# Optimization experiments

Measured on AMD Instinct MI355X. Metric: run time of the kernel, lower is better.

## Reference

```python
import jax, jax.numpy as jnp
import numpy as np

B, S, H = 2, 2048, 2048
NH, NKV, D = 16, 4, 128
E, K, F = 16, 2, 768
EPS = 1e-6
THETA = 1e6


def setup_inputs() -> dict:
    key = jax.random.key(0)
    ks = jax.random.split(key, 10)
    sd = 0.02
    rn = lambda k, shp: jax.random.normal(k, shp, jnp.float32) * sd
    return {
        "positions": jnp.arange(S, dtype=jnp.int32),
        "hidden_states": jax.random.normal(ks[0], (B, S, H), jnp.float32),
        "residual": jax.random.normal(ks[1], (B, S, H), jnp.float32),
        "w_in_ln": jnp.ones((H,), jnp.float32),
        "wq": rn(ks[2], (H, NH * D)),
        "wk": rn(ks[3], (H, NKV * D)),
        "wv": rn(ks[4], (H, NKV * D)),
        "wo": rn(ks[5], (NH * D, H)),
        "q_norm_w": jnp.ones((D,), jnp.float32),
        "k_norm_w": jnp.ones((D,), jnp.float32),
        "w_post_ln": jnp.ones((H,), jnp.float32),
        "gate_w": rn(ks[6], (H, E)),
        "w_gate_up": rn(ks[7], (E, H, 2 * F)),
        "w_down": rn(ks[8], (E, F, H)),
    }


def _rmsnorm(x, w):
    return x * jax.lax.rsqrt(jnp.mean(x * x, axis=-1, keepdims=True) + EPS) * w


def _rope(x, positions):
    # x: [B, S, h, D], neox-style rotate-half RoPE
    half = D // 2
    inv_freq = 1.0 / (THETA ** (jnp.arange(half, dtype=jnp.float32) / half))
    ang = positions.astype(jnp.float32)[:, None] * inv_freq  # [S, half]
    cos = jnp.cos(ang)[None, :, None, :]
    sin = jnp.sin(ang)[None, :, None, :]
    x1, x2 = x[..., :half], x[..., half:]
    return jnp.concatenate([x1 * cos - x2 * sin, x2 * cos + x1 * sin], axis=-1)


def reference(positions, hidden_states, residual, w_in_ln, wq, wk, wv, wo,
              q_norm_w, k_norm_w, w_post_ln, gate_w, w_gate_up, w_down):
    # fused RMSNorm + residual (residual is not None branch)
    residual = hidden_states + residual
    h = _rmsnorm(residual, w_in_ln)

    # --- Qwen3 attention: qk-norm + RoPE + causal GQA ---
    q = _rmsnorm((h @ wq).reshape(B, S, NH, D), q_norm_w)
    k = _rmsnorm((h @ wk).reshape(B, S, NKV, D), k_norm_w)
    v = (h @ wv).reshape(B, S, NKV, D)
    q = _rope(q, positions)
    k = _rope(k, positions)
    rep = NH // NKV
    k = jnp.repeat(k, rep, axis=2)
    v = jnp.repeat(v, rep, axis=2)
    scores = jnp.einsum('bqhd,bkhd->bhqk', q, k) / np.sqrt(D).astype(np.float32)
    causal = jnp.tril(jnp.ones((S, S), bool))
    scores = jnp.where(causal, scores, -jnp.inf)
    attn = jax.nn.softmax(scores, axis=-1)
    o = jnp.einsum('bhqk,bkhd->bqhd', attn, v).reshape(B, S, NH * D) @ wo

    # fused RMSNorm + residual
    residual = o + residual
    h = _rmsnorm(residual, w_post_ln)

    # --- MoE: top-k router (renormalized) + capacity-based grouped GEMM dispatch ---
    x = h.reshape(-1, H)                      # [T, H]
    T = B * S
    probs = jax.nn.softmax((x @ gate_w).astype(jnp.float32), axis=-1)
    tw, tids = jax.lax.top_k(probs, K)        # [T, K]
    tw = (tw / tw.sum(axis=-1, keepdims=True)).astype(x.dtype)

    P = T * K
    C = (2 * P) // E
    eids = tids.reshape(-1)                   # [P]
    oneh = jax.nn.one_hot(eids, E, dtype=jnp.int32)
    pos_in_e = (jnp.cumsum(oneh, axis=0) * oneh).sum(-1) - 1   # slot within expert
    valid = pos_in_e < C
    pos_c = jnp.minimum(pos_in_e, C - 1)
    e_safe = jnp.where(valid, eids, E)        # overflow -> dump row E

    xr = jnp.repeat(x, K, axis=0)             # [P, H]
    buf = jnp.zeros((E + 1, C, H), x.dtype).at[e_safe, pos_c].set(xr)[:E]
    gu = jnp.einsum('ech,ehf->ecf', buf, w_gate_up)            # [E, C, 2F]
    g, u = jnp.split(gu, 2, axis=-1)
    dn = jnp.einsum('ecf,efh->ech', jax.nn.silu(g) * u, w_down)
    dn = jnp.concatenate([dn, jnp.zeros((1, C, H), dn.dtype)], axis=0)
    yp = dn[e_safe, pos_c] * tw.reshape(-1)[:, None]           # [P, H]
    y = yp.reshape(T, K, H).sum(axis=1)
    return y.reshape(B, S, H), residual
```

## Files before the change

### kernel.cpp

```cpp
#include <hip/hip_runtime.h>
#include <stdint.h>

#define T_TOK 4096
#define HDIM  2048
#define SEQ   2048
#define NHQ   16
#define NKVH  4
#define DH    128
#define NE    16
#define CCAP  1024
#define FF    768
#define EPSF  1e-6f

typedef __attribute__((ext_vector_type(4))) float          f32x4;
typedef __attribute__((ext_vector_type(8))) _Float16       f16x8;
typedef __attribute__((ext_vector_type(4))) unsigned short u16x4;
typedef __attribute__((ext_vector_type(8))) unsigned short u16x8;

__device__ __forceinline__ unsigned short f2h(float f){ return __builtin_bit_cast(unsigned short, (_Float16)f); }
__device__ __forceinline__ float h2f(unsigned short u){ return (float)__builtin_bit_cast(_Float16, u); }
__device__ __forceinline__ void split2(float x, unsigned short& hi, unsigned short& lo){
  unsigned short h = f2h(x);
  hi = h; lo = f2h((x - h2f(h)) * 4096.f);
}
__device__ __forceinline__ void gl_lds16(const void* g, void* l){
  __builtin_amdgcn_global_load_lds((const __attribute__((address_space(1))) unsigned int*)g,
                                   (__attribute__((address_space(3))) unsigned int*)l, 16, 0, 0);
}
__device__ __forceinline__ int bswz(int row){ return ((row & 7) ^ ((row >> 3) & 7)) << 3; }

__global__ __launch_bounds__(256) void k_addnorm(
    const float* __restrict__ hs, const float* __restrict__ rs, const float* __restrict__ w,
    float* __restrict__ resid, unsigned short* __restrict__ hhi, unsigned short* __restrict__ hlo)
{
  int t = blockIdx.x, tid = threadIdx.x;
  size_t off = (size_t)t * HDIM;
  float4 a0 = ((const float4*)(hs+off))[tid];
  float4 b0 = ((const float4*)(rs+off))[tid];
  float4 a1 = ((const float4*)(hs+off))[tid+256];
  float4 b1 = ((const float4*)(rs+off))[tid+256];
  float4 s0 = make_float4(a0.x+b0.x, a0.y+b0.y, a0.z+b0.z, a0.w+b0.w);
  float4 s1 = make_float4(a1.x+b1.x, a1.y+b1.y, a1.z+b1.z, a1.w+b1.w);
  float ssq = s0.x*s0.x+s0.y*s0.y+s0.z*s0.z+s0.w*s0.w
            + s1.x*s1.x+s1.y*s1.y+s1.z*s1.z+s1.w*s1.w;
  #pragma unroll
  for (int sh=1; sh<64; sh<<=1) ssq += __shfl_xor(ssq, sh);
  __shared__ float red[4];
  if ((tid & 63) == 0) red[tid>>6] = ssq;
  __syncthreads();
  float tot = red[0]+red[1]+red[2]+red[3];
  float r = 1.f / sqrtf(tot * (1.f/HDIM) + EPSF);
  ((float4*)(resid+off))[tid]     = s0;
  ((float4*)(resid+off))[tid+256] = s1;
  float4 w0 = ((const float4*)w)[tid];
  float4 w1 = ((const float4*)w)[tid+256];
  u16x4 hv, lv; unsigned short ta, tb;
  split2(s0.x*r*w0.x, ta, tb); hv.x=ta; lv.x=tb;
  split2(s0.y*r*w0.y, ta, tb); hv.y=ta; lv.y=tb;
  split2(s0.z*r*w0.z, ta, tb); hv.z=ta; lv.z=tb;
  split2(s0.w*r*w0.w, ta, tb); hv.w=ta; lv.w=tb;
  ((u16x4*)(hhi+off))[tid] = hv; ((u16x4*)(hlo+off))[tid] = lv;
  split2(s1.x*r*w1.x, ta, tb); hv.x=ta; lv.x=tb;
  split2(s1.y*r*w1.y, ta, tb); hv.y=ta; lv.y=tb;
  split2(s1.z*r*w1.z, ta, tb); hv.z=ta; lv.z=tb;
  split2(s1.w*r*w1.w, ta, tb); hv.w=ta; lv.w=tb;
  ((u16x4*)(hhi+off))[tid+256] = hv; ((u16x4*)(hlo+off))[tid+256] = lv;
}

__global__ void k_cstab(const int* __restrict__ pos, float* __restrict__ cs)
{
  int i = blockIdx.x*256 + threadIdx.x;
  if (i >= SEQ*64) return;
  int s = i >> 6, f = i & 63;
  float pw  = (float)exp((double)f * 13.815510557964274 / 64.0);
  float inv = 1.0f / pw;
  float ang = (float)pos[s] * inv;
  float sv, cv;
  sincosf(ang, &sv, &cv);
  ((float2*)cs)[i] = make_float2(cv, sv);
}

__global__ __launch_bounds__(256) void k_normrope(
    unsigned short* __restrict__ qh, unsigned short* __restrict__ ql,
    unsigned short* __restrict__ kh, unsigned short* __restrict__ kl,
    const float* __restrict__ qnw, const float* __restrict__ knw,
    const float* __restrict__ cs)
{
  int t = blockIdx.x, head = blockIdx.y*4 + (threadIdx.x>>6), lane = threadIdx.x & 63;
  int s = t & (SEQ-1);
  unsigned short *dh, *dl; const float* wn; float scale; size_t off;
  if (head < NHQ){ off = ((size_t)t*NHQ + head)*DH; dh = qh+off; dl = ql+off; wn = qnw; scale = 0.08838834764831845f; }
  else           { off = ((size_t)t*NKVH + (head-NHQ))*DH; dh = kh+off; dl = kl+off; wn = knw; scale = 1.f; }
  float x1 = h2f(dh[lane])    + h2f(dl[lane])   *(1.f/4096.f);
  float x2 = h2f(dh[lane+64]) + h2f(dl[lane+64])*(1.f/4096.f);
  float ssq = x1*x1 + x2*x2;
  #pragma unroll
  for (int sh=1; sh<64; sh<<=1) ssq += __shfl_xor(ssq, sh);
  float r = 1.f / sqrtf(ssq * (1.f/DH) + EPSF);
  float y1 = x1*r*wn[lane], y2 = x2*r*wn[lane+64];
  float2 csp = ((const float2*)cs)[s*64 + lane];
  float o1 = (y1*csp.x - y2*csp.y) * scale;
  float o2 = (y2*csp.x + y1*csp.y) * scale;
  unsigned short a, b;
  split2(o1, a, b); dh[lane]    = a; dl[lane]    = b;
  split2(o2, a, b); dh[lane+64] = a; dl[lane+64] = b;
}

__global__ __launch_bounds__(256) void k_wsplit(
    const float* __restrict__ W, int Kd, int Ncols,
    unsigned short* __restrict__ Whi, unsigned short* __restrict__ Wlo)
{
  int k0 = blockIdx.x*64, n0 = blockIdx.y*64;
  __shared__ float T[64][65];
  int tid = threadIdx.x;
  int tr = tid >> 4;
  int tc = (tid & 15) * 4;
  #pragma unroll
  for (int i=0;i<4;i++){
    int k = tr + i*16;
    float4 v = *(const float4*)(W + (size_t)(k0 + k)*Ncols + n0 + tc);
    T[k][tc+0]=v.x; T[k][tc+1]=v.y; T[k][tc+2]=v.z; T[k][tc+3]=v.w;
  }
  __syncthreads();
  int n  = tid >> 2;
  int kc = (tid & 3) * 16;
  u16x8 hv0, lv0, hv1, lv1;
  #pragma unroll
  for (int j=0;j<8;j++){
    unsigned short hi, lo; split2(T[kc+j][n], hi, lo);
    hv0[j]=hi; lv0[j]=lo;
  }
  #pragma unroll
  for (int j=0;j<8;j++){
    unsigned short hi, lo; split2(T[kc+8+j][n], hi, lo);
    hv1[j]=hi; lv1[j]=lo;
  }
  size_t ob = (size_t)(n0 + n)*Kd + k0 + kc;
  *(u16x8*)(Whi + ob)     = hv0;
  *(u16x8*)(Whi + ob + 8) = hv1;
  *(u16x8*)(Wlo + ob)     = lv0;
  *(u16x8*)(Wlo + ob + 8) = lv1;
}

__global__ __launch_bounds__(256,2) void k_gemm_qkv(
    const unsigned short* __restrict__ Ahi, const unsigned short* __restrict__ Alo,
    const unsigned short* __restrict__ Whi, const unsigned short* __restrict__ Wlo,
    unsigned short* __restrict__ qh, unsigned short* __restrict__ ql,
    unsigned short* __restrict__ kh, unsigned short* __restrict__ kl,
    unsigned short* __restrict__ vh, unsigned short* __restrict__ vl)
{
  const int Kd = HDIM;
  int bm = blockIdx.x, bn2 = blockIdx.y;
  int bn, N, noff; unsigned short *Ch, *Cl;
  if (bn2 < 16){ bn = bn2;      N = 2048; noff = 0;    Ch = qh; Cl = ql; }
  else if (bn2 < 20){ bn = bn2-16; N = 512; noff = 2048; Ch = kh; Cl = kl; }
  else { bn = bn2-20; N = 512; noff = 2560; Ch = vh; Cl = vl; }

  __shared__ unsigned short As[2][8192];
  __shared__ unsigned short Bs[2][8192];

  int tid = threadIdx.x, lane = tid & 63, w = tid >> 6;
  int wr = w >> 1, wc = w & 1;

  size_t arow_g[4], brow_g[4];
  int lb_[4];
  #pragma unroll
  for (int i=0;i<4;i++){
    int ob = w*4096 + i*1024 + lane*16;
    int row = ob >> 7;
    int colB = ob & 127;
    int scolB = colB ^ ((row & 7) << 4);
    arow_g[i] = (size_t)(bm*128 + row) * Kd + (scolB >> 1);
    brow_g[i] = (size_t)(noff + bn*128 + row) * Kd + (scolB >> 1);
    lb_[i] = (w*4096 + i*1024) >> 1;
  }

  f32x4 accA[4][4] = {};
  f32x4 accB[4][4] = {};

  for (int kt = 0; kt < Kd/64; kt++){
    #pragma unroll
    for (int i=0;i<4;i++){
      gl_lds16(Ahi + arow_g[i] + kt*64, (void*)&As[0][lb_[i]]);
      gl_lds16(Alo + arow_g[i] + kt*64, (void*)&As[1][lb_[i]]);
      gl_lds16(Whi + brow_g[i] + kt*64, (void*)&Bs[0][lb_[i]]);
      gl_lds16(Wlo + brow_g[i] + kt*64, (void*)&Bs[1][lb_[i]]);
    }
    __syncthreads();
    #pragma unroll
    for (int kk=0; kk<2; kk++){
      f16x8 ah[4], al[4], bh[4], bl[4];
      #pragma unroll
      for (int m=0;m<4;m++){
        int row = wr*64 + m*16 + (lane & 15);
        int ci = (kk*32 + ((lane>>4)<<3)) ^ ((row & 7) << 3);
        ah[m] = *(const f16x8*)&As[0][row*64 + ci];
        al[m] = *(const f16x8*)&As[1][row*64 + ci];
      }
      #pragma unroll
      for (int n=0;n<4;n++){
        int row = wc*64 + n*16 + (lane & 15);
        int ci = (kk*32 + ((lane>>4)<<3)) ^ ((row & 7) << 3);
        bh[n] = *(const f16x8*)&Bs[0][row*64 + ci];
        bl[n] = *(const f16x8*)&Bs[1][row*64 + ci];
      }
      #pragma unroll
      for (int m=0;m<4;m++)
        #pragma unroll
        for (int n=0;n<4;n++){
          accA[m][n] = __builtin_amdgcn_mfma_f32_16x16x32_f16(ah[m], bh[n], accA[m][n], 0,0,0);
          accB[m][n] = __builtin_amdgcn_mfma_f32_16x16x32_f16(ah[m], bl[n], accB[m][n], 0,0,0);
          accB[m][n] = __builtin_amdgcn_mfma_f32_16x16x32_f16(al[m], bh[n], accB[m][n], 0,0,0);
        }
    }
    __syncthreads();
  }
  int r0 = (lane >> 4) << 2, c0 = lane & 15;
  #pragma unroll
  for (int m=0;m<4;m++){
    int grow0 = bm*128 + wr*64 + m*16 + r0;
    #pragma unroll
    for (int n=0;n<4;n++){
      int gcol = bn*128 + wc*64 + n*16 + c0;
      #pragma unroll
      for (int j=0;j<4;j++){
        float v = accA[m][n][j] + accB[m][n][j] * (1.f/4096.f);
        int grow = grow0 + j;
        unsigned short hi, lo; split2(v, hi, lo);
        Ch[(size_t)grow*N + gcol] = hi;
        Cl[(size_t)grow*N + gcol] = lo;
      }
    }
  }
}

template<int MODE>
__global__ __launch_bounds__(256,2) void k_gemm(
    const unsigned short* __restrict__ Ahi, const unsigned short* __restrict__ Alo,
    const float* __restrict__ Bsrc,
    const unsigned short* __restrict__ Bhi, const unsigned short* __restrict__ Blo,
    void* __restrict__ C1,
    int N, int Kd,
    const int* __restrict__ erow, const int* __restrict__ counts,
    const float* __restrict__ topw)
{
  constexpr int SPLIT = (MODE <= 2) ? 1 : 0;
  int bm = blockIdx.x, bn = blockIdx.y, e = blockIdx.z;
  int cnt = 0;
  const unsigned short* Abase = Ahi;
  const float* Bp = Bsrc;
  if constexpr (MODE == 3){ cnt = counts[e]; if (bm*128 >= cnt) return; Bp = Bsrc + (size_t)e*Kd*N; }
  if constexpr (MODE == 4){ cnt = counts[e]; if (bm*128 >= cnt) return; Bp = Bsrc + (size_t)e*Kd*N; Abase = Ahi + (size_t)e*CCAP*Kd; }

  __shared__ unsigned short As[SPLIT?2:1][8192];
  __shared__ unsigned short Bs[SPLIT?2:1][8192];

  int tid = threadIdx.x, lane = tid & 63, w = tid >> 6;
  int wr = w >> 1, wc = w & 1;

  size_t arow_g[4], brow_g[4];
  int lb_[4];
  #pragma unroll
  for (int i=0;i<4;i++){
    int ob = w*4096 + i*1024 + lane*16;
    int row = ob >> 7;
    int colB = ob & 127;
    int scolB = colB ^ ((row & 7) << 4);
    int grow;
    if constexpr (MODE == 3){
      grow = erow[e*CCAP + bm*128 + row] >> 1;
    } else {
      grow = bm*128 + row;
    }
    arow_g[i] = (size_t)grow * Kd + (scolB >> 1);
    brow_g[i] = (size_t)(bn*128 + row) * Kd + (scolB >> 1);
    lb_[i] = (w*4096 + i*1024) >> 1;
  }

  f32x4 accA[4][4] = {};
  f32x4 accB[4][4] = {};

  int nK = Kd >> 6;
  for (int kt = 0; kt < nK; kt++){
    #pragma unroll
    for (int i=0;i<4;i++){
      gl_lds16(Abase + arow_g[i] + kt*64, (void*)&As[0][lb_[i]]);
      if constexpr (SPLIT) gl_lds16(Alo + arow_g[i] + kt*64, (void*)&As[1][lb_[i]]);
    }
    if constexpr (SPLIT){
      #pragma unroll
      for (int i=0;i<4;i++){
        gl_lds16(Bhi + brow_g[i] + kt*64, (void*)&Bs[0][lb_[i]]);
        gl_lds16(Blo + brow_g[i] + kt*64, (void*)&Bs[1][lb_[i]]);
      }
    } else {
      #pragma unroll
      for (int it=0; it<2; it++){
        int b2 = tid + it*256;
        int k0 = (b2 >> 5) << 2;
        int n0 = (b2 & 31) << 2;
        const float* bp = Bp + (size_t)(kt*64 + k0)*N + bn*128 + n0;
        float4 f0 = *(const float4*)bp;
        float4 f1 = *(const float4*)(bp + (size_t)N);
        float4 f2 = *(const float4*)(bp + 2*(size_t)N);
        float4 f3 = *(const float4*)(bp + 3*(size_t)N);
        #define DO_COL(J, CX) { \
          int rown = n0 + J; \
          int idx = rown*64 + (k0 ^ bswz(rown)); \
          u16x4 ph; ph.x=f2h(f0.CX); ph.y=f2h(f1.CX); ph.z=f2h(f2.CX); ph.w=f2h(f3.CX); \
          *(u16x4*)&Bs[0][idx] = ph; }
        DO_COL(0, x) DO_COL(1, y) DO_COL(2, z) DO_COL(3, w)
        #undef DO_COL
      }
    }
    __syncthreads();
    #pragma unroll
    for (int kk=0; kk<2; kk++){
      f16x8 ah[4], al[4], bh[4], bl[4];
      #pragma unroll
      for (int m=0;m<4;m++){
        int row = wr*64 + m*16 + (lane & 15);
        int ci = (kk*32 + ((lane>>4)<<3)) ^ ((row & 7) << 3);
        ah[m] = *(const f16x8*)&As[0][row*64 + ci];
        if constexpr (SPLIT) al[m] = *(const f16x8*)&As[1][row*64 + ci];
      }
      #pragma unroll
      for (int n=0;n<4;n++){
        int row = wc*64 + n*16 + (lane & 15);
        int sw = SPLIT ? ((row & 7) << 3) : bswz(row);
        int ci = (kk*32 + ((lane>>4)<<3)) ^ sw;
        bh[n] = *(const f16x8*)&Bs[0][row*64 + ci];
        if constexpr (SPLIT) bl[n] = *(const f16x8*)&Bs[1][row*64 + ci];
      }
      #pragma unroll
      for (int m=0;m<4;m++)
        #pragma unroll
        for (int n=0;n<4;n++){
          accA[m][n] = __builtin_amdgcn_mfma_f32_16x16x32_f16(ah[m], bh[n], accA[m][n], 0,0,0);
          if constexpr (SPLIT){
            accB[m][n] = __builtin_amdgcn_mfma_f32_16x16x32_f16(ah[m], bl[n], accB[m][n], 0,0,0);
            accB[m][n] = __builtin_amdgcn_mfma_f32_16x16x32_f16(al[m], bh[n], accB[m][n], 0,0,0);
          }
        }
    }
    __syncthreads();
  }
  int r0 = (lane >> 4) << 2, c0 = lane & 15;
  #pragma unroll
  for (int m=0;m<4;m++){
    int grow0 = bm*128 + wr*64 + m*16 + r0;
    #pragma unroll
    for (int n=0;n<4;n++){
      int gcol = bn*128 + wc*64 + n*16 + c0;
      #pragma unroll
      for (int j=0;j<4;j++){
        float v = accA[m][n][j];
        if constexpr (SPLIT) v += accB[m][n][j] * (1.f/4096.f);
        int grow = grow0 + j;
        if constexpr (MODE == 2){
          size_t idx = (size_t)grow*N + gcol;
          ((float*)C1)[idx] += v;
        } else if constexpr (MODE == 3){
          ((unsigned short*)C1)[((size_t)e*CCAP + grow)*N + gcol] = f2h(v);
        } else if constexpr (MODE == 4){
          if (grow < cnt){
            int p = erow[e*CCAP + grow];
            ((float*)C1)[(size_t)p*N + gcol] = v;
          }
        }
      }
    }
  }
}

__global__ __launch_bounds__(512,2) void k_attn(
    const unsigned short* __restrict__ qh, const unsigned short* __restrict__ ql,
    const unsigned short* __restrict__ kh, const unsigned short* __restrict__ kl,
    const unsigned short* __restrict__ vh, const unsigned short* __restrict__ vl,
    unsigned short* __restrict__ oh, unsigned short* __restrict__ ol)
{
  int h = blockIdx.y, b = blockIdx.z;
  int qt = b ? (15 - blockIdx.x) : blockIdx.x;
  int hkv = h >> 2;
  int tid = threadIdx.x, lane = tid & 63, w = tid >> 6;

  __shared__ unsigned short Ks[2][2][8192];
  __shared__ unsigned short Vs[2][2][8192];
  __shared__ unsigned short Ps[8][2][1024];

  int qrow = qt*128 + w*16 + (lane & 15);
  size_t qoff = ((size_t)(b*SEQ + qrow)*NHQ + h)*DH + ((lane>>4)<<3);
  f16x8 qfh[4], qfl[4];
  #pragma unroll
  for (int kk=0; kk<4; kk++){
    qfh[kk] = *(const f16x8*)(qh + qoff + kk*32);
    qfl[kk] = *(const f16x8*)(ql + qoff + kk*32);
  }

  const size_t SROW = (size_t)NKVH*DH;
  size_t kvbase = (size_t)b*SEQ*SROW + (size_t)hkv*DH;
  int kob[2]; size_t koff[2];
  #pragma unroll
  for (int i=0;i<2;i++){
    int ob = i*8192 + tid*16;
    int row = ob >> 8;
    int scol = (ob & 255) ^ ((row & 7) << 4);
    kob[i] = ob;
    koff[i] = (size_t)row*SROW + (scol >> 1);
  }
  int vkvp = (tid & 31) * 2;
  int vd0  = ((tid >> 5) & 15) * 8;
  size_t voff0 = (size_t)vkvp*SROW + vd0;
  size_t voff1 = voff0 + SROW;

  u16x8 pkh[2], pkl[2];
  u16x8 pvh[2], pvl[2];

  #define STAGE_LOAD(KVT) { \
    size_t tb = kvbase + (size_t)(KVT)*64*SROW; \
    _Pragma("unroll") \
    for (int i=0;i<2;i++){ pkh[i] = *(const u16x8*)(kh + tb + koff[i]); \
                           pkl[i] = *(const u16x8*)(kl + tb + koff[i]); } \
    pvh[0] = *(const u16x8*)(vh + tb + voff0); \
    pvh[1] = *(const u16x8*)(vh + tb + voff1); \
    pvl[0] = *(const u16x8*)(vl + tb + voff0); \
    pvl[1] = *(const u16x8*)(vl + tb + voff1); }

  #define STAGE_WRITE(BUF) { \
    _Pragma("unroll") \
    for (int i=0;i<2;i++){ \
      *(u16x8*)((char*)&Ks[BUF][0][0] + kob[i]) = pkh[i]; \
      *(u16x8*)((char*)&Ks[BUF][1][0] + kob[i]) = pkl[i]; } \
    _Pragma("unroll") \
    for (int jj=0;jj<8;jj++){ \
      int row = vd0 + jj; \
      int idx = row*64 + (vkvp ^ ((jj & 7) << 3)); \
      *(unsigned int*)&Vs[BUF][0][idx] = (unsigned int)pvh[0][jj] | ((unsigned int)pvh[1][jj] << 16); \
      *(unsigned int*)&Vs[BUF][1][idx] = (unsigned int)pvl[0][jj] | ((unsigned int)pvl[1][jj] << 16); } }

  #define QKT(KVT, BUF) { \
    f32x4 saA[4] = {}; \
    f32x4 saB[4] = {}; \
    __builtin_amdgcn_s_setprio(1); \
    _Pragma("unroll") \
    for (int kk=0; kk<4; kk++){ \
      _Pragma("unroll") \
      for (int n=0;n<4;n++){ \
        int row = n*16 + (lane & 15); \
        int ci = (kk*32 + ((lane>>4)<<3)) ^ ((row & 7) << 3); \
        f16x8 kfh = *(const f16x8*)&Ks[BUF][0][row*128 + ci]; \
        f16x8 kfl = *(const f16x8*)&Ks[BUF][1][row*128 + ci]; \
        saA[n] = __builtin_amdgcn_mfma_f32_16x16x32_f16(qfh[kk], kfh, saA[n], 0,0,0); \
        saB[n] = __builtin_amdgcn_mfma_f32_16x16x32_f16(qfh[kk], kfl, saB[n], 0,0,0); \
        saB[n] = __builtin_amdgcn_mfma_f32_16x16x32_f16(qfl[kk], kfh, saB[n], 0,0,0); } } \
    __builtin_amdgcn_s_setprio(0); \
    _Pragma("unroll") \
    for (int j=0;j<4;j++) mx[j] = -1e30f; \
    int qg = qt*128 + w*16 + ((lane>>4)<<2); \
    _Pragma("unroll") \
    for (int n=0;n<4;n++){ \
      int kvcol = (KVT)*64 + n*16 + (lane & 15); \
      _Pragma("unroll") \
      for (int j=0;j<4;j++){ \
        float sv = saA[n][j] + saB[n][j]*(1.f/4096.f); \
        if (kvcol > qg + j) sv = -1e30f; \
        p[n][j] = sv; \
        mx[j] = fmaxf(mx[j], sv); } } }

  #define SOFTMAX() { \
    _Pragma("unroll") \
    for (int sh=1; sh<16; sh<<=1) \
      _Pragma("unroll") \
      for (int j=0;j<4;j++) mx[j] = fmaxf(mx[j], __shfl_xor(mx[j], sh)); \
    float rs[4], sum[4]; \
    _Pragma("unroll") \
    for (int j=0;j<4;j++){ \
      float mn = fmaxf(m_[j], mx[j]); \
      rs[j] = __expf(m_[j] - mn); \
      float sm = 0.f; \
      _Pragma("unroll") \
      for (int n=0;n<4;n++){ float pe = __expf(p[n][j] - mn); p[n][j] = pe; sm += pe; } \
      sum[j] = sm; \
      m_[j] = mn; } \
    _Pragma("unroll") \
    for (int sh=1; sh<16; sh<<=1) \
      _Pragma("unroll") \
      for (int j=0;j<4;j++) sum[j] += __shfl_xor(sum[j], sh); \
    _Pragma("unroll") \
    for (int j=0;j<4;j++) l_[j] = l_[j]*rs[j] + sum[j]; \
    _Pragma("unroll") \
    for (int d=0;d<8;d++) \
      _Pragma("unroll") \
      for (int j=0;j<4;j++){ oaccA[d][j] *= rs[j]; oaccB[d][j] *= rs[j]; } \
    _Pragma("unroll") \
    for (int n=0;n<4;n++) \
      _Pragma("unroll") \
      for (int j=0;j<4;j++){ \
        int r = ((lane>>4)<<2) + j; \
        int c = n*16 + (lane & 15); \
        int idx = r*64 + (c ^ ((r & 7) << 3)); \
        unsigned short ph, pl2; split2(p[n][j], ph, pl2); \
        Ps[w][0][idx] = ph; \
        Ps[w][1][idx] = pl2; } }

  #define PVOP(BUF) { \
    __builtin_amdgcn_s_setprio(1); \
    _Pragma("unroll") \
    for (int kk=0; kk<2; kk++){ \
      int prow = lane & 15; \
      int pidx = prow*64 + ((kk*32 + ((lane>>4)<<3)) ^ ((prow & 7) << 3)); \
      f16x8 pah = *(const f16x8*)&Ps[w][0][pidx]; \
      f16x8 pal = *(const f16x8*)&Ps[w][1][pidx]; \
      _Pragma("unroll") \
      for (int d=0;d<8;d++){ \
        int row = d*16 + (lane & 15); \
        int ci = (kk*32 + ((lane>>4)<<3)) ^ ((row & 7) << 3); \
        f16x8 vfh = *(const f16x8*)&Vs[BUF][0][row*64 + ci]; \
        f16x8 vfl = *(const f16x8*)&Vs[BUF][1][row*64 + ci]; \
        oaccA[d] = __builtin_amdgcn_mfma_f32_16x16x32_f16(pah, vfh, oaccA[d], 0,0,0); \
        oaccB[d] = __builtin_amdgcn_mfma_f32_16x16x32_f16(pah, vfl, oaccB[d], 0,0,0); \
        oaccB[d] = __builtin_amdgcn_mfma_f32_16x16x32_f16(pal, vfh, oaccB[d], 0,0,0); } } \
    __builtin_amdgcn_s_setprio(0); }

  float m_[4], l_[4];
  f32x4 oaccA[8] = {};
  f32x4 oaccB[8] = {};
  #pragma unroll
  for (int j=0;j<4;j++){ m_[j] = -1e30f; l_[j] = 0.f; }

  int nkt = 2*qt + 2;
  STAGE_LOAD(0); STAGE_WRITE(0);
  STAGE_LOAD(1); STAGE_WRITE(1);
  __syncthreads();

  float p[4][4], mx[4];
  QKT(0, 0);

  for (int kvt = 0; kvt < nkt; kvt++){
    int cur = kvt & 1, nxt = cur ^ 1;
    if (kvt+2 < nkt) STAGE_LOAD(kvt+2);

    bool active = (kvt*64 <= qt*128 + w*16 + 15);
    bool actn   = (kvt+1 < nkt) && ((kvt+1)*64 <= qt*128 + w*16 + 15);
    if (actn){
      SOFTMAX();
      QKT(kvt+1, nxt);
      PVOP(cur);
    } else if (active){
      SOFTMAX();
      PVOP(cur);
    }
    __syncthreads();
    if (kvt+2 < nkt) STAGE_WRITE(cur);
    __syncthreads();
  }
  #undef STAGE_LOAD
  #undef STAGE_WRITE
  #undef QKT
  #undef SOFTMAX
  #undef PVOP

  #pragma unroll
  for (int j=0;j<4;j++) l_[j] = 1.f / l_[j];
  #pragma unroll
  for (int d=0;d<8;d++)
    #pragma unroll
    for (int j=0;j<4;j++){
      int qr = qt*128 + w*16 + ((lane>>4)<<2) + j;
      size_t off = ((size_t)(b*SEQ + qr)*NHQ + h)*DH + d*16 + (lane & 15);
      float v = (oaccA[d][j] + oaccB[d][j]*(1.f/4096.f)) * l_[j];
      unsigned short hi, lo; split2(v, hi, lo);
      oh[off] = hi; ol[off] = lo;
    }
}

__global__ __launch_bounds__(256) void k_ln2gate(
    const float* __restrict__ resid, const float* __restrict__ wln,
    const float* __restrict__ gw,
    unsigned short* __restrict__ x2, float* __restrict__ topw, int* __restrict__ topid)
{
  int t = blockIdx.x, tid = threadIdx.x;
  size_t off = (size_t)t * HDIM;
  float4 s0 = ((const float4*)(resid+off))[tid];
  float4 s1 = ((const float4*)(resid+off))[tid+256];
  float ssq = s0.x*s0.x+s0.y*s0.y+s0.z*s0.z+s0.w*s0.w
            + s1.x*s1.x+s1.y*s1.y+s1.z*s1.z+s1.w*s1.w;
  #pragma unroll
  for (int sh=1; sh<64; sh<<=1) ssq += __shfl_xor(ssq, sh);
  __shared__ float red[4];
  if ((tid & 63) == 0) red[tid>>6] = ssq;
  __syncthreads();
  float tot = red[0]+red[1]+red[2]+red[3];
  float r = 1.f / sqrtf(tot * (1.f/HDIM) + EPSF);
  float4 w0 = ((const float4*)wln)[tid];
  float4 w1 = ((const float4*)wln)[tid+256];
  float xs[8] = { s0.x*r*w0.x, s0.y*r*w0.y, s0.z*r*w0.z, s0.w*r*w0.w,
                  s1.x*r*w1.x, s1.y*r*w1.y, s1.z*r*w1.z, s1.w*r*w1.w };
  u16x4 hv;
  hv.x = f2h(xs[0]); hv.y = f2h(xs[1]); hv.z = f2h(xs[2]); hv.w = f2h(xs[3]);
  ((u16x4*)(x2+off))[tid] = hv;
  hv.x = f2h(xs[4]); hv.y = f2h(xs[5]); hv.z = f2h(xs[6]); hv.w = f2h(xs[7]);
  ((u16x4*)(x2+off))[tid+256] = hv;

  double acc[16];
  #pragma unroll
  for (int e2=0;e2<16;e2++) acc[e2] = 0.0;
  #pragma unroll
  for (int i=0;i<8;i++){
    int hidx = (i<4) ? (tid*4 + i) : (1024 + tid*4 + (i-4));
    const float4* g4 = (const float4*)(gw + (size_t)hidx*NE);
    float4 ga=g4[0], gb=g4[1], gc=g4[2], gd=g4[3];
    double xx = (double)xs[i];
    acc[0]+=xx*ga.x;  acc[1]+=xx*ga.y;  acc[2]+=xx*ga.z;  acc[3]+=xx*ga.w;
    acc[4]+=xx*gb.x;  acc[5]+=xx*gb.y;  acc[6]+=xx*gb.z;  acc[7]+=xx*gb.w;
    acc[8]+=xx*gc.x;  acc[9]+=xx*gc.y;  acc[10]+=xx*gc.z; acc[11]+=xx*gc.w;
    acc[12]+=xx*gd.x; acc[13]+=xx*gd.y; acc[14]+=xx*gd.z; acc[15]+=xx*gd.w;
  }
  __shared__ double red2[256][16];
  #pragma unroll
  for (int e2=0;e2<16;e2++) red2[tid][e2] = acc[e2];
  __syncthreads();
  for (int s=128; s>=1; s>>=1){
    if (tid < s){
      #pragma unroll
      for (int e2=0;e2<16;e2++) red2[tid][e2] += red2[tid+s][e2];
    }
    __syncthreads();
  }
  if (tid == 0){
    float l[16];
    #pragma unroll
    for (int e2=0;e2<16;e2++) l[e2] = (float)red2[0][e2];
    int i0 = 0;
    #pragma unroll
    for (int e2=1;e2<16;e2++) if (l[e2] > l[i0]) i0 = e2;
    int i1 = (i0 == 0) ? 1 : 0;
    #pragma unroll
    for (int e2=0;e2<16;e2++) if (e2 != i0 && l[e2] > l[i1]) i1 = e2;
    float w0t = 1.f / (1.f + expf(l[i1] - l[i0]));
    topw[t*2+0] = w0t; topw[t*2+1] = 1.f - w0t;
    topid[t*2+0] = i0; topid[t*2+1] = i1;
  }
}

__global__ __launch_bounds__(256) void k_route(
    int* __restrict__ topid, int* __restrict__ erow, int* __restrict__ counts)
{
  int tid = threadIdx.x;
  __shared__ unsigned short cnt[256][16];
  for (int i = tid; i < NE*CCAP; i += 256) erow[i] = 0;
  int loc[16];
  #pragma unroll
  for (int e2=0;e2<16;e2++) loc[e2] = 0;
  int myid[32];
  for (int i=0;i<32;i++){
    int e2 = topid[tid*32 + i];
    myid[i] = e2;
    loc[e2]++;
  }
  #pragma unroll
  for (int e2=0;e2<16;e2++) cnt[tid][e2] = (unsigned short)loc[e2];
  __syncthreads();
  if (tid < 16){
    int run = 0;
    for (int i=0;i<256;i++){ int c = cnt[i][tid]; cnt[i][tid] = (unsigned short)run; run += c; }
    counts[tid] = run > CCAP ? CCAP : run;
  }
  __syncthreads();
  #pragma unroll
  for (int e2=0;e2<16;e2++) loc[e2] = cnt[tid][e2];
  for (int i=0;i<32;i++){
    int e2 = myid[i];
    int pos = loc[e2]++;
    int p = tid*32 + i;
    int ok = (pos < CCAP);
    if (ok) erow[e2*CCAP + pos] = p;
    topid[p] = ok;
  }
}

__global__ void k_silu(const unsigned short* __restrict__ gu, unsigned short* __restrict__ act)
{
  int idx = blockIdx.x*256 + threadIdx.x;
  int nrow = idx / 96;
  int fo = (idx - nrow*96) * 8;
  const unsigned short* gr = gu + (size_t)nrow*1536;
  u16x8 g = *(const u16x8*)(gr + fo);
  u16x8 u = *(const u16x8*)(gr + 768 + fo);
  u16x8 o;
  #pragma unroll
  for (int i=0;i<8;i++){
    float gf = h2f(g[i]), uf = h2f(u[i]);
    float s = gf / (1.f + __expf(-gf));
    o[i] = f2h(s * uf);
  }
  *(u16x8*)(act + (size_t)nrow*768 + fo) = o;
}

__global__ __launch_bounds__(256) void k_gather(
    const float* __restrict__ yp, const int* __restrict__ valid,
    const float* __restrict__ topw, float* __restrict__ y)
{
  int t = blockIdx.x, tid = threadIdx.x;
  int v0 = valid[t*2+0], v1 = valid[t*2+1];
  float w0 = topw[t*2+0], w1 = topw[t*2+1];
  size_t o = (size_t)t*2*HDIM;
  const float4* r0 = (const float4*)(yp + o);
  const float4* r1 = (const float4*)(yp + o + HDIM);
  float4* yo = (float4*)(y + (size_t)t*HDIM);
  #pragma unroll
  for (int i=0;i<2;i++){
    int ix = tid + i*256;
    float4 a = r0[ix];
    float4 b = r1[ix];
    float4 out;
    float a0 = v0 ? w0 : 0.f;
    float b0 = v1 ? w1 : 0.f;
    out.x = (v0 ? a.x*a0 : 0.f) + (v1 ? b.x*b0 : 0.f);
    out.y = (v0 ? a.y*a0 : 0.f) + (v1 ? b.y*b0 : 0.f);
    out.z = (v0 ? a.z*a0 : 0.f) + (v1 ? b.z*b0 : 0.f);
    out.w = (v0 ? a.w*a0 : 0.f) + (v1 ? b.w*b0 : 0.f);
    yo[ix] = out;
  }
}

extern "C" void kernel_launch(void* const* d_in, const int* in_sizes, int n_in,
                              void* d_out, int out_size, void* d_ws, size_t ws_size,
                              hipStream_t stream)
{
  (void)in_sizes; (void)n_in; (void)out_size; (void)ws_size;
  const int*   positions = (const int*)  d_in[0];
  const float* hs        = (const float*)d_in[1];
  const float* res       = (const float*)d_in[2];
  const float* w_in_ln   = (const float*)d_in[3];
  const float* wq        = (const float*)d_in[4];
  const float* wk        = (const float*)d_in[5];
  const float* wv        = (const float*)d_in[6];
  const float* wo        = (const float*)d_in[7];
  const float* q_norm_w  = (const float*)d_in[8];
  const float* k_norm_w  = (const float*)d_in[9];
  const float* w_post_ln = (const float*)d_in[10];
  const float* gate_w    = (const float*)d_in[11];
  const float* w_gate_up = (const float*)d_in[12];
  const float* w_down    = (const float*)d_in[13];

  float* y      = (float*)d_out;
  float* resid2 = y + (size_t)T_TOK*HDIM;

  char* ws = (char*)d_ws;
  unsigned short* hhi = (unsigned short*)(ws + 0);
  unsigned short* hlo = (unsigned short*)(ws + 16777216);
  unsigned short* qh  = (unsigned short*)(ws + 33554432);
  unsigned short* ql  = (unsigned short*)(ws + 50331648);
  unsigned short* kh  = (unsigned short*)(ws + 67108864);
  unsigned short* kl  = (unsigned short*)(ws + 71303168);
  unsigned short* vh  = (unsigned short*)(ws + 75497472);
  unsigned short* vl  = (unsigned short*)(ws + 79691776);
  unsigned short* oh  = (unsigned short*)(ws + 83886080);
  unsigned short* ol  = (unsigned short*)(ws + 100663296);
  unsigned short* x2  = (unsigned short*)(ws + 117440512);
  unsigned short* qkvwh = (unsigned short*)(ws + 83886080);
  unsigned short* qkvwl = (unsigned short*)(ws + 96468992);
  unsigned short* wowh  = (unsigned short*)(ws + 117440512);
  unsigned short* wowl  = (unsigned short*)(ws + 125829120);
  unsigned short* gu  = (unsigned short*)(ws + 0);
  unsigned short* act = (unsigned short*)(ws + 67108864);
  float*          yp  = (float*)         (ws + 0);
  float* cstab        = (float*)(ws + 134217728);
  float* topw         = (float*)(ws + 135266304);
  int*   topid        = (int*)  (ws + 135299072);
  int*   counts       = (int*)  (ws + 135331840);
  int*   erow         = (int*)  (ws + 135332096);

  k_addnorm<<<T_TOK, 256, 0, stream>>>(hs, res, w_in_ln, resid2, hhi, hlo);
  k_cstab<<<(SEQ*64 + 255)/256, 256, 0, stream>>>(positions, cstab);
  k_wsplit<<<dim3(32, 32), 256, 0, stream>>>(wq, HDIM, 2048, qkvwh,                     qkvwl);
  k_wsplit<<<dim3(32,  8), 256, 0, stream>>>(wk, HDIM,  512, qkvwh + (size_t)2048*HDIM, qkvwl + (size_t)2048*HDIM);
  k_wsplit<<<dim3(32,  8), 256, 0, stream>>>(wv, HDIM,  512, qkvwh + (size_t)2560*HDIM, qkvwl + (size_t)2560*HDIM);
  k_wsplit<<<dim3(32, 32), 256, 0, stream>>>(wo, HDIM, 2048, wowh,                      wowl);
  k_gemm_qkv<<<dim3(32,24,1), 256, 0, stream>>>(hhi, hlo, qkvwh, qkvwl, qh, ql, kh, kl, vh, vl);
  k_normrope<<<dim3(T_TOK, 5), 256, 0, stream>>>(qh, ql, kh, kl, q_norm_w, k_norm_w, cstab);
  k_attn<<<dim3(16, 16, 2), 512, 0, stream>>>(qh, ql, kh, kl, vh, vl, oh, ol);
  k_gemm<2><<<dim3(32,16,1), 256, 0, stream>>>(oh, ol, nullptr, wowh, wowl, resid2, 2048, 2048, nullptr, nullptr, nullptr);
  k_ln2gate<<<T_TOK, 256, 0, stream>>>(resid2, w_post_ln, gate_w, x2, topw, topid);
  k_route<<<1, 256, 0, stream>>>(topid, erow, counts);
  k_gemm<3><<<dim3(8,12,16), 256, 0, stream>>>(x2, nullptr, w_gate_up, nullptr, nullptr, gu, 1536, 2048, erow, counts, nullptr);
  k_silu<<<6144, 256, 0, stream>>>(gu, act);
  k_gemm<4><<<dim3(8,16,16), 256, 0, stream>>>(act, nullptr, w_down, nullptr, nullptr, yp, 2048, 768, erow, counts, nullptr);
  k_gather<<<T_TOK, 256, 0, stream>>>(yp, topid, topw, y);
}
```

Baseline: 1.051 ms.

## Fuse SiLU into expert gate/up GEMM and restage attention K/V writes

Adds a dedicated gate/up expert GEMM that computes the gate and up tiles in the same block, applies SiLU*up in the epilogue, and writes the activation directly. This removes the separate SiLU kernel and the round trip of the intermediate gate/up buffer through memory. Each block now holds two accumulator sets and an extra shared buffer, which may cut occupancy. Separately, the attention loop splits the K and V shared-memory staging writes and moves the K write ahead of compute to drop one barrier per iteration. That reordering adds a risk of a shared-buffer race.

After: 1.050 ms. About the same (-0.1%).

```diff
diff --git a/kernel.cpp b/kernel.cpp
--- a/kernel.cpp
+++ b/kernel.cpp
@@ -249,7 +249,6 @@
   int cnt = 0;
   const unsigned short* Abase = Ahi;
   const float* Bp = Bsrc;
-  if constexpr (MODE == 3){ cnt = counts[e]; if (bm*128 >= cnt) return; Bp = Bsrc + (size_t)e*Kd*N; }
   if constexpr (MODE == 4){ cnt = counts[e]; if (bm*128 >= cnt) return; Bp = Bsrc + (size_t)e*Kd*N; Abase = Ahi + (size_t)e*CCAP*Kd; }
 
   __shared__ unsigned short As[SPLIT?2:1][8192];
@@ -266,12 +265,7 @@
     int row = ob >> 7;
     int colB = ob & 127;
     int scolB = colB ^ ((row & 7) << 4);
-    int grow;
-    if constexpr (MODE == 3){
-      grow = erow[e*CCAP + bm*128 + row] >> 1;
-    } else {
-      grow = bm*128 + row;
-    }
+    int grow = bm*128 + row;
     arow_g[i] = (size_t)grow * Kd + (scolB >> 1);
     brow_g[i] = (size_t)(bn*128 + row) * Kd + (scolB >> 1);
     lb_[i] = (w*4096 + i*1024) >> 1;
@@ -360,8 +354,6 @@
         if constexpr (MODE == 2){
           size_t idx = (size_t)grow*N + gcol;
           ((float*)C1)[idx] += v;
-        } else if constexpr (MODE == 3){
-          ((unsigned short*)C1)[((size_t)e*CCAP + grow)*N + gcol] = f2h(v);
         } else if constexpr (MODE == 4){
           if (grow < cnt){
             int p = erow[e*CCAP + grow];
@@ -373,6 +365,116 @@
   }
 }
 
+__global__ __launch_bounds__(256,2) void k_gemm_gu(
+    const unsigned short* __restrict__ Ahi,
+    const float* __restrict__ Bsrc,
+    unsigned short* __restrict__ act,
+    const int* __restrict__ erow, const int* __restrict__ counts)
+{
+  const int Kd = HDIM, N = 1536;
+  int bm = blockIdx.x, bn = blockIdx.y, e = blockIdx.z;
+  int cnt = counts[e]; if (bm*128 >= cnt) return;
+  const float* Bp = Bsrc + (size_t)e*Kd*N;
+
+  __shared__ unsigned short As [8192];
+  __shared__ unsigned short BsG[8192];
+  __shared__ unsigned short BsU[8192];
+
+  int tid = threadIdx.x, lane = tid & 63, w = tid >> 6;
+  int wr = w >> 1, wc = w & 1;
+
+  size_t arow_g[4];
+  int lb_[4];
+  #pragma unroll
+  for (int i=0;i<4;i++){
+    int ob = w*4096 + i*1024 + lane*16;
+    int row = ob >> 7;
+    int colB = ob & 127;
+    int scolB = colB ^ ((row & 7) << 4);
+    int grow = erow[e*CCAP + bm*128 + row] >> 1;
+    arow_g[i] = (size_t)grow * Kd + (scolB >> 1);
+    lb_[i] = (w*4096 + i*1024) >> 1;
+  }
+
+  f32x4 accG[4][4] = {};
+  f32x4 accU[4][4] = {};
+
+  for (int kt = 0; kt < Kd/64; kt++){
+    #pragma unroll
+    for (int i=0;i<4;i++)
+      gl_lds16(Ahi + arow_g[i] + kt*64, (void*)&As[lb_[i]]);
+    #pragma unroll
+    for (int it=0; it<2; it++){
+      int b2 = tid + it*256;
+      int k0 = (b2 >> 5) << 2;
+      int n0 = (b2 & 31) << 2;
+      const float* bpg = Bp + (size_t)(kt*64 + k0)*N + bn*128 + n0;
+      const float* bpu = bpg + 768;
+      float4 g0 = *(const float4*)bpg;
+      float4 g1 = *(const float4*)(bpg + (size_t)N);
+      float4 g2 = *(const float4*)(bpg + 2*(size_t)N);
+      float4 g3 = *(const float4*)(bpg + 3*(size_t)N);
+      float4 u0 = *(const float4*)bpu;
+      float4 u1 = *(const float4*)(bpu + (size_t)N);
+      float4 u2 = *(const float4*)(bpu + 2*(size_t)N);
+      float4 u3 = *(const float4*)(bpu + 3*(size_t)N);
+      #define DO_COL2(J, CX) { \
+        int rown = n0 + J; \
+        int idx = rown*64 + (k0 ^ bswz(rown)); \
+        u16x4 pg; pg.x=f2h(g0.CX); pg.y=f2h(g1.CX); pg.z=f2h(g2.CX); pg.w=f2h(g3.CX); \
+        *(u16x4*)&BsG[idx] = pg; \
+        u16x4 pu; pu.x=f2h(u0.CX); pu.y=f2h(u1.CX); pu.z=f2h(u2.CX); pu.w=f2h(u3.CX); \
+        *(u16x4*)&BsU[idx] = pu; }
+      DO_COL2(0, x) DO_COL2(1, y) DO_COL2(2, z) DO_COL2(3, w)
+      #undef DO_COL2
+    }
+    __syncthreads();
+    #pragma unroll
+    for (int kk=0; kk<2; kk++){
+      f16x8 ah[4], bg[4], bu[4];
+      #pragma unroll
+      for (int m=0;m<4;m++){
+        int row = wr*64 + m*16 + (lane & 15);
+        int ci = (kk*32 + ((lane>>4)<<3)) ^ ((row & 7) << 3);
+        ah[m] = *(const f16x8*)&As[row*64 + ci];
+      }
+      #pragma unroll
+      for (int n=0;n<4;n++){
+        int row = wc*64 + n*16 + (lane & 15);
+        int ci = (kk*32 + ((lane>>4)<<3)) ^ bswz(row);
+        bg[n] = *(const f16x8*)&BsG[row*64 + ci];
+        bu[n] = *(const f16x8*)&BsU[row*64 + ci];
+      }
+      #pragma unroll
+      for (int m=0;m<4;m++)
+        #pragma unroll
+        for (int n=0;n<4;n++){
+          accG[m][n] = __builtin_amdgcn_mfma_f32_16x16x32_f16(ah[m], bg[n], accG[m][n], 0,0,0);
+          accU[m][n] = __builtin_amdgcn_mfma_f32_16x16x32_f16(ah[m], bu[n], accU[m][n], 0,0,0);
+        }
+    }
+    __syncthreads();
+  }
+  int r0 = (lane >> 4) << 2, c0 = lane & 15;
+  #pragma unroll
+  for (int m=0;m<4;m++){
+    int grow0 = bm*128 + wr*64 + m*16 + r0;
+    #pragma unroll
+    for (int n=0;n<4;n++){
+      int gcol = bn*128 + wc*64 + n*16 + c0;
+      #pragma unroll
+      for (int j=0;j<4;j++){
+        int grow = grow0 + j;
+        unsigned short g16 = f2h(accG[m][n][j]);
+        unsigned short u16_ = f2h(accU[m][n][j]);
+        float gf = h2f(g16), uf = h2f(u16_);
+        float s = gf / (1.f + __expf(-gf));
+        act[((size_t)e*CCAP + grow)*FF + gcol] = f2h(s * uf);
+      }
+    }
+  }
+}
+
 __global__ __launch_bounds__(512,2) void k_attn(
     const unsigned short* __restrict__ qh, const unsigned short* __restrict__ ql,
     const unsigned short* __restrict__ kh, const unsigned short* __restrict__ kl,
@@ -426,11 +528,13 @@
     pvl[0] = *(const u16x8*)(vl + tb + voff0); \
     pvl[1] = *(const u16x8*)(vl + tb + voff1); }
 
-  #define STAGE_WRITE(BUF) { \
+  #define STAGE_WRITE_K(BUF) { \
     _Pragma("unroll") \
     for (int i=0;i<2;i++){ \
       *(u16x8*)((char*)&Ks[BUF][0][0] + kob[i]) = pkh[i]; \
-      *(u16x8*)((char*)&Ks[BUF][1][0] + kob[i]) = pkl[i]; } \
+      *(u16x8*)((char*)&Ks[BUF][1][0] + kob[i]) = pkl[i]; } }
+
+  #define STAGE_WRITE_V(BUF) { \
     _Pragma("unroll") \
     for (int jj=0;jj<8;jj++){ \
       int row = vd0 + jj; \
@@ -529,8 +633,8 @@
   for (int j=0;j<4;j++){ m_[j] = -1e30f; l_[j] = 0.f; }
 
   int nkt = 2*qt + 2;
-  STAGE_LOAD(0); STAGE_WRITE(0);
-  STAGE_LOAD(1); STAGE_WRITE(1);
+  STAGE_LOAD(0); STAGE_WRITE_K(0); STAGE_WRITE_V(0);
+  STAGE_LOAD(1); STAGE_WRITE_K(1); STAGE_WRITE_V(1);
   __syncthreads();
 
   float p[4][4], mx[4];
@@ -538,8 +642,11 @@
 
   for (int kvt = 0; kvt < nkt; kvt++){
     int cur = kvt & 1, nxt = cur ^ 1;
-    if (kvt+2 < nkt) STAGE_LOAD(kvt+2);
-
+    bool h2 = (kvt+2 < nkt);
+    if (h2){
+      STAGE_LOAD(kvt+2);
+      if (kvt) STAGE_WRITE_K(cur);
+    }
     bool active = (kvt*64 <= qt*128 + w*16 + 15);
     bool actn   = (kvt+1 < nkt) && ((kvt+1)*64 <= qt*128 + w*16 + 15);
     if (actn){
@@ -551,11 +658,14 @@
       PVOP(cur);
     }
     __syncthreads();
-    if (kvt+2 < nkt) STAGE_WRITE(cur);
-    __syncthreads();
+    if (h2){
+      if (!kvt){ STAGE_WRITE_K(cur); __syncthreads(); }
+      STAGE_WRITE_V(cur);
+    }
   }
   #undef STAGE_LOAD
-  #undef STAGE_WRITE
+  #undef STAGE_WRITE_K
+  #undef STAGE_WRITE_V
   #undef QKT
   #undef SOFTMAX
   #undef PVOP
@@ -677,24 +787,6 @@
     if (ok) erow[e2*CCAP + pos] = p;
     topid[p] = ok;
   }
-}
-
-__global__ void k_silu(const unsigned short* __restrict__ gu, unsigned short* __restrict__ act)
-{
-  int idx = blockIdx.x*256 + threadIdx.x;
-  int nrow = idx / 96;
-  int fo = (idx - nrow*96) * 8;
-  const unsigned short* gr = gu + (size_t)nrow*1536;
-  u16x8 g = *(const u16x8*)(gr + fo);
-  u16x8 u = *(const u16x8*)(gr + 768 + fo);
-  u16x8 o;
-  #pragma unroll
-  for (int i=0;i<8;i++){
-    float gf = h2f(g[i]), uf = h2f(u[i]);
-    float s = gf / (1.f + __expf(-gf));
-    o[i] = f2h(s * uf);
-  }
-  *(u16x8*)(act + (size_t)nrow*768 + fo) = o;
 }
 
 __global__ __launch_bounds__(256) void k_gather(
@@ -763,7 +855,6 @@
   unsigned short* qkvwl = (unsigned short*)(ws + 96468992);
   unsigned short* wowh  = (unsigned short*)(ws + 117440512);
   unsigned short* wowl  = (unsigned short*)(ws + 125829120);
-  unsigned short* gu  = (unsigned short*)(ws + 0);
   unsigned short* act = (unsigned short*)(ws + 67108864);
   float*          yp  = (float*)         (ws + 0);
   float* cstab        = (float*)(ws + 134217728);
@@ -784,8 +875,7 @@
   k_gemm<2><<<dim3(32,16,1), 256, 0, stream>>>(oh, ol, nullptr, wowh, wowl, resid2, 2048, 2048, nullptr, nullptr, nullptr);
   k_ln2gate<<<T_TOK, 256, 0, stream>>>(resid2, w_post_ln, gate_w, x2, topw, topid);
   k_route<<<1, 256, 0, stream>>>(topid, erow, counts);
-  k_gemm<3><<<dim3(8,12,16), 256, 0, stream>>>(x2, nullptr, w_gate_up, nullptr, nullptr, gu, 1536, 2048, erow, counts, nullptr);
-  k_silu<<<6144, 256, 0, stream>>>(gu, act);
+  k_gemm_gu<<<dim3(8,6,16), 256, 0, stream>>>(x2, w_gate_up, act, erow, counts);
   k_gemm<4><<<dim3(8,16,16), 256, 0, stream>>>(act, nullptr, w_down, nullptr, nullptr, yp, 2048, 768, erow, counts, nullptr);
   k_gather<<<T_TOK, 256, 0, stream>>>(yp, topid, topw, y);
 }
```
